# Kernel tuning notes

Hardware: AMD Instinct MI355X
Metric: run time of the kernel (lower is better)

## Reference

```python
import jax, jax.numpy as jnp
import numpy as np

HEADS = 8

def setup_inputs() -> dict:
    key = jax.random.key(0)
    ks = jax.random.split(key, 10)
    B, C, D, W, H = 4, 256, 12, 12, 12
    dk = C // HEADS
    return {
        "x": jax.random.normal(ks[0], (B, C, D, W, H), jnp.float32),
        "wq": jax.random.normal(ks[1], (C, C), jnp.float32) * 0.05,
        "bq": jax.random.normal(ks[2], (C,), jnp.float32) * 0.05,
        "wk": jax.random.normal(ks[3], (C, C), jnp.float32) * 0.05,
        "bk": jax.random.normal(ks[4], (C,), jnp.float32) * 0.05,
        "wv": jax.random.normal(ks[5], (C, C), jnp.float32) * 0.05,
        "bv": jax.random.normal(ks[6], (C,), jnp.float32) * 0.05,
        "rel_d": jax.random.normal(ks[7], (1, HEADS, dk, D, 1, 1), jnp.float32),
        "rel_h": jax.random.normal(ks[8], (1, HEADS, dk, 1, 1, H), jnp.float32),
        "rel_w": jax.random.normal(ks[9], (1, HEADS, dk, 1, W, 1), jnp.float32),
    }


def reference(x, wq, bq, wk, bk, wv, bv, rel_d, rel_h, rel_w):
    B, C, D, W, H = x.shape
    dk = C // HEADS
    N = D * W * H

    def proj(w, b):
        # Conv3d kernel_size=1 == per-voxel linear over channels
        y = jnp.einsum('bcdwh,oc->bodwh', x, w) + b[None, :, None, None, None]
        return y.reshape(B, HEADS, dk, N)  # [B,h,dk,N]

    q = proj(wq, bq)
    k = proj(wk, bk)
    v = proj(wv, bv)

    # content-content: q^T k -> [B,h,N,N]
    cc = jnp.einsum('bhdn,bhdm->bhnm', q, k)
    # relative-position bias: (rel_h+rel_w+rel_d) broadcasts to [1,h,dk,D,W,H]
    pos = (rel_h + rel_w + rel_d).reshape(1, HEADS, dk, N)
    # content-position: pos^T @ q -> [B,h,N,N]
    cp = jnp.einsum('bhdn,bhdm->bhnm', pos, q)

    attn = jax.nn.softmax(cc + cp, axis=-1)  # [B,h,N,N]
    # out = v @ attn^T -> [B,h,dk,N]
    out = jnp.einsum('bhdn,bhmn->bhdm', v, attn)
    return out.reshape(B, C, D, W, H)
```

## Files before the change

kernel.cpp:

```cpp
#include <hip/hip_runtime.h>
#include <math.h>

#define HEADS 8
#define DK 32
#define B_ 4
#define C_ 256
#define NVOX 1728
#define DE 64
#define PITCH 72
#define XPITCH 136
#define CPITCH 36
#define LOG2E 1.44269504088896f

typedef _Float16 f16x8 __attribute__((ext_vector_type(8)));
typedef __fp16 fp16x2 __attribute__((ext_vector_type(2)));
typedef float f32x16 __attribute__((ext_vector_type(16)));

__device__ inline float h2f(short s) {
    _Float16 h = *(_Float16*)&s;
    return (float)h;
}
__device__ inline f32x16 mfma32h(f16x8 a, f16x8 b, f32x16 c) {
    return __builtin_amdgcn_mfma_f32_32x32x16_f16(a, b, c, 0, 0, 0);
}

union H8 { _Float16 h[8]; uint4 v; };
union H4 { _Float16 h[4]; uint2 v; };

__global__ __launch_bounds__(256)
void prep_kernel(const float* __restrict__ x,
                 const float* __restrict__ wq, const float* __restrict__ wk,
                 const float* __restrict__ wv,
                 const float* __restrict__ rel_d, const float* __restrict__ rel_h,
                 const float* __restrict__ rel_w,
                 short* __restrict__ wf, short* __restrict__ xf,
                 short* __restrict__ Qf) {
    __shared__ float tile[64][65];
    int bid = blockIdx.x;
    int t = threadIdx.x;

    if (bid < 192) {
        int idx = (bid * 256 + t) * 4;
        int m = idx >> 16;
        const float* w = (m == 0) ? wq : (m == 1) ? wk : wv;
        float4 v = *(const float4*)&w[idx & 65535];
        H4 hh;
        hh.h[0] = (_Float16)v.x; hh.h[1] = (_Float16)v.y;
        hh.h[2] = (_Float16)v.z; hh.h[3] = (_Float16)v.w;
        *(uint2*)&wf[idx] = hh.v;
    } else if (bid < 624) {
        int q = bid - 192;
        int nb = (q % 27) * 64;
        int c0 = ((q / 27) % 4) * 64;
        int b  = q / 108;
        const float* xb = x + (size_t)b * C_ * NVOX;
        for (int e = t; e < 4096; e += 256) {
            int ci = e >> 6, nl = e & 63;
            tile[ci][nl] = xb[(size_t)(c0 + ci) * NVOX + nb + nl];
        }
        __syncthreads();
        for (int e = t; e < 512; e += 256) {
            int n = e >> 3, cg = (e & 7) * 8;
            H8 hi;
            #pragma unroll
            for (int j = 0; j < 8; j++) hi.h[j] = (_Float16)tile[cg + j][n];
            *(uint4*)&xf[((size_t)b * NVOX + nb + n) * C_ + c0 + cg] = hi.v;
        }
    } else {
        int q = bid - 624;
        int nb = (q % 27) * 64;
        int h  = (q / 27) % 8;
        int b  = q / 216;
        int bh = b * HEADS + h;
        int nl = t & 63, dd0 = (t >> 6) * 8;
        int n = nb + nl;
        int di = n / 144, wi = (n / 12) % 12, hi = n % 12;
        H8 ph;
        #pragma unroll
        for (int o = 0; o < 8; o++) {
            int hd = h * DK + dd0 + o;
            ph.h[o] = (_Float16)(rel_d[hd * 12 + di] + rel_w[hd * 12 + wi] +
                                 rel_h[hd * 12 + hi]);
        }
        *(uint4*)&Qf[((size_t)bh * NVOX + n) * DE + DK + dd0] = ph.v;
    }
}

struct FS {
    union {
        short xs[64 * XPITCH];
        float cbuf[3][64][CPITCH];
    } u;
};

__global__ __launch_bounds__(384, 4)
void fproj_kernel(const short* __restrict__ xf, const short* __restrict__ wf,
                  const float* __restrict__ bq, const float* __restrict__ bk,
                  const float* __restrict__ bv,
                  short* __restrict__ Qf, short* __restrict__ Kf,
                  short* __restrict__ Vf) {
    __shared__ FS sm;
    int nb = blockIdx.x * 64, h = blockIdx.y, b = blockIdx.z;
    int bh = b * HEADS + h;
    int t = threadIdx.x;
    int w = t >> 6, l = t & 63, ln = l & 31, hv = l >> 5;
    int mat = w >> 1, nh = w & 1;

    const short* xb = xf + ((size_t)b * NVOX + nb) * C_;
    const short* wA = wf + ((size_t)mat * C_ + h * DK + ln) * C_;
    int xrow = (nh * 32 + ln) * XPITCH;

    f32x16 acc;
    #pragma unroll
    for (int r = 0; r < 16; r++) acc[r] = 0.f;

    #pragma unroll 1
    for (int ch = 0; ch < 2; ch++) {
        __syncthreads();
        for (int e = t; e < 1024; e += 384) {
            int row = e >> 4, c8 = (e & 15) * 8;
            *(uint4*)&sm.u.xs[row * XPITCH + c8] =
                *(const uint4*)&xb[row * C_ + ch * 128 + c8];
        }
        __syncthreads();
        #pragma unroll 4
        for (int ks = 0; ks < 8; ks++) {
            int kl_ = ks * 16 + hv * 8;
            f16x8 a = *(const f16x8*)&wA[ch * 128 + kl_];
            f16x8 bfr = *(const f16x8*)&sm.u.xs[xrow + kl_];
            acc = mfma32h(a, bfr, acc);
        }
    }
    __syncthreads();

    const float* bias = (mat == 0) ? bq : (mat == 1) ? bk : bv;
    int ncol = nh * 32 + ln;
    #pragma unroll
    for (int q2 = 0; q2 < 4; q2++) {
        float4 cv;
        float* cvp = (float*)&cv;
        #pragma unroll
        for (int m = 0; m < 4; m++) {
            int o_loc = 8 * q2 + 4 * hv + m;
            cvp[m] = acc[4 * q2 + m] + bias[h * DK + o_loc];
        }
        *(float4*)&sm.u.cbuf[mat][ncol][8 * q2 + 4 * hv] = cv;
    }
    __syncthreads();

    if (t < 256) {
        int n = t >> 2, ddg = (t & 3) * 8;
        size_t rowoff = ((size_t)bh * NVOX + nb + n) * DE;
        H8 qh, kh;
        #pragma unroll
        for (int j = 0; j < 8; j++) {
            qh.h[j] = (_Float16)sm.u.cbuf[0][n][ddg + j];
            kh.h[j] = (_Float16)sm.u.cbuf[1][n][ddg + j];
        }
        *(uint4*)&Qf[rowoff + ddg] = qh.v;
        *(uint4*)&Kf[rowoff + ddg] = kh.v;
        *(uint4*)&Kf[rowoff + DK + ddg] = qh.v;
    }
    if (t < 256) {
        int d = t >> 3, ng = (t & 7) * 8;
        H8 vv;
        #pragma unroll
        for (int j = 0; j < 8; j++)
            vv.h[j] = (_Float16)sm.u.cbuf[2][ng + j][d];
        *(uint4*)&Vf[((size_t)bh * DK + d) * NVOX + nb + ng] = vv.v;
    }
}

struct SMem {
    short K[64][PITCH];
    short V[DK][PITCH];
    short P[64][PITCH];
};

__global__ __launch_bounds__(128, 3)
void attn_kernel(const short* __restrict__ Qf, const short* __restrict__ Kf,
                 const short* __restrict__ Vf,
                 short* __restrict__ wsO, float* __restrict__ wsM,
                 float* __restrict__ wsL) {
    __shared__ SMem sm;
    int bx = blockIdx.x;
    int it = bx >> 1, jp = bx & 1;
    int h = blockIdx.y, b = blockIdx.z;
    int bh = b * HEADS + h;
    int t = threadIdx.x;
    int w  = t >> 6;
    int l  = t & 63;
    int ln = l & 31;
    int hv = l >> 5;
    int i_loc  = w * 32 + ln;
    int i_glob = it * 64 + i_loc;

    const short* Qp = Qf + (size_t)bh * NVOX * DE;
    const short* Kp = Kf + (size_t)bh * NVOX * DE;
    const short* Vp = Vf + (size_t)bh * DK * NVOX;

    f16x8 qf[4];
    #pragma unroll
    for (int ks = 0; ks < 4; ks++)
        qf[ks] = *(const f16x8*)&Qp[(size_t)i_glob * DE + ks * 16 + hv * 8];

    float mL = -INFINITY;
    float lsum = 0.f;
    f32x16 O;
    #pragma unroll
    for (int r = 0; r < 16; r++) O[r] = 0.f;

    int krow0 = t >> 3, kcol = (t & 7) * 8;
    int vrow0 = t >> 3;
    uint4 kr[4], vr[2];

    int jt0 = jp ? 14 : 0, jt1 = jp ? 27 : 14;

    {
        int jb = jt0 * 64;
        #pragma unroll
        for (int q = 0; q < 4; q++)
            kr[q] = *(const uint4*)&Kp[(size_t)(jb + krow0 + q * 16) * DE + kcol];
        #pragma unroll
        for (int q = 0; q < 2; q++)
            vr[q] = *(const uint4*)&Vp[(size_t)(vrow0 + q * 16) * NVOX + jb + kcol];
        #pragma unroll
        for (int q = 0; q < 4; q++)
            *(uint4*)&sm.K[krow0 + q * 16][kcol] = kr[q];
        #pragma unroll
        for (int q = 0; q < 2; q++)
            *(uint4*)&sm.V[vrow0 + q * 16][kcol] = vr[q];
    }

    #pragma unroll 1
    for (int jt = jt0; jt < jt1; jt++) {
        __syncthreads();
        bool more = (jt + 1 < jt1);
        if (more) {
            int jb = (jt + 1) * 64;
            #pragma unroll
            for (int q = 0; q < 4; q++)
                kr[q] = *(const uint4*)&Kp[(size_t)(jb + krow0 + q * 16) * DE + kcol];
            #pragma unroll
            for (int q = 0; q < 2; q++)
                vr[q] = *(const uint4*)&Vp[(size_t)(vrow0 + q * 16) * NVOX + jb + kcol];
        }

        f32x16 sc[2];
        #pragma unroll
        for (int js = 0; js < 2; js++) {
            f32x16 s;
            #pragma unroll
            for (int r = 0; r < 16; r++) s[r] = 0.f;
            #pragma unroll
            for (int ks = 0; ks < 4; ks++) {
                f16x8 kfr = *(const f16x8*)&sm.K[js * 32 + ln][ks * 16 + hv * 8];
                s = mfma32h(kfr, qf[ks], s);
            }
            sc[js] = s;
        }

        float mx = sc[0][0];
        #pragma unroll
        for (int js = 0; js < 2; js++)
            #pragma unroll
            for (int r = 0; r < 16; r++) mx = fmaxf(mx, sc[js][r]);
        mx = fmaxf(mx, __shfl_xor(mx, 32));
        float mLn = fmaxf(mL, mx * LOG2E);
        float alpha = exp2f(mL - mLn);
        mL = mLn;
        float ps = 0.f;
        #pragma unroll
        for (int js = 0; js < 2; js++)
            #pragma unroll
            for (int r = 0; r < 16; r++) {
                float p = exp2f(fmaf(sc[js][r], LOG2E, -mLn));
                sc[js][r] = p;
                ps += p;
            }
        ps += __shfl_xor(ps, 32);
        lsum = lsum * alpha + ps;

        #pragma unroll
        for (int js = 0; js < 2; js++)
            #pragma unroll
            for (int g = 0; g < 4; g++) {
                union { fp16x2 h2[2]; uint2 v; } pk;
                pk.h2[0] = __builtin_amdgcn_cvt_pkrtz(sc[js][4 * g + 0], sc[js][4 * g + 1]);
                pk.h2[1] = __builtin_amdgcn_cvt_pkrtz(sc[js][4 * g + 2], sc[js][4 * g + 3]);
                *(uint2*)&sm.P[i_loc][js * 32 + g * 8 + hv * 4] = pk.v;
            }

        #pragma unroll
        for (int r = 0; r < 16; r++) O[r] *= alpha;
        #pragma unroll
        for (int ks = 0; ks < 4; ks++) {
            f16x8 va = *(const f16x8*)&sm.V[ln][ks * 16 + hv * 8];
            f16x8 pb = *(const f16x8*)&sm.P[i_loc][ks * 16 + hv * 8];
            O = mfma32h(va, pb, O);
        }

        __syncthreads();
        if (more) {
            #pragma unroll
            for (int q = 0; q < 4; q++)
                *(uint4*)&sm.K[krow0 + q * 16][kcol] = kr[q];
            #pragma unroll
            for (int q = 0; q < 2; q++)
                *(uint4*)&sm.V[vrow0 + q * 16][kcol] = vr[q];
        }
    }

    short* Op = wsO + ((size_t)jp * (B_ * HEADS) + bh) * DK * NVOX;
    #pragma unroll
    for (int r = 0; r < 16; r++) {
        int d = (r & 3) + 8 * (r >> 2) + 4 * hv;
        _Float16 oh = (_Float16)O[r];
        Op[(size_t)d * NVOX + i_glob] = *(short*)&oh;
    }
    if (hv == 0) {
        size_t mo = ((size_t)jp * (B_ * HEADS) + bh) * NVOX + i_glob;
        wsM[mo] = mL;
        wsL[mo] = lsum;
    }
}

__global__ void combine_kernel(const short* __restrict__ wsO,
                               const float* __restrict__ wsM,
                               const float* __restrict__ wsL,
                               float* __restrict__ out) {
    int idx = (blockIdx.x * 256 + threadIdx.x) * 4;
    int i = idx % NVOX;
    int bh = (idx / NVOX) >> 5;
    const size_t oh = (size_t)B_ * HEADS * DK * NVOX;
    const size_t mh = (size_t)B_ * HEADS * NVOX;
    size_t mo = (size_t)bh * NVOX + i;
    float4 m0 = *(const float4*)&wsM[mo];
    float4 m1 = *(const float4*)&wsM[mh + mo];
    float4 l0 = *(const float4*)&wsL[mo];
    float4 l1 = *(const float4*)&wsL[mh + mo];
    uint2 o0u = *(const uint2*)&wsO[idx];
    uint2 o1u = *(const uint2*)&wsO[oh + idx];
    const short* o0s = (const short*)&o0u;
    const short* o1s = (const short*)&o1u;
    const float* m0p = (const float*)&m0; const float* m1p = (const float*)&m1;
    const float* l0p = (const float*)&l0; const float* l1p = (const float*)&l1;
    float4 res;
    float* rp = (float*)&res;
    #pragma unroll
    for (int j = 0; j < 4; j++) {
        float m = fmaxf(m0p[j], m1p[j]);
        float a0 = exp2f(m0p[j] - m), a1 = exp2f(m1p[j] - m);
        rp[j] = (a0 * h2f(o0s[j]) + a1 * h2f(o1s[j])) /
                (a0 * l0p[j] + a1 * l1p[j]);
    }
    *(float4*)&out[idx] = res;
}

extern "C" void kernel_launch(void* const* d_in, const int* in_sizes, int n_in,
                              void* d_out, int out_size, void* d_ws, size_t ws_size,
                              hipStream_t stream) {
    const float* x     = (const float*)d_in[0];
    const float* wq    = (const float*)d_in[1];
    const float* bq    = (const float*)d_in[2];
    const float* wk    = (const float*)d_in[3];
    const float* bk    = (const float*)d_in[4];
    const float* wv    = (const float*)d_in[5];
    const float* bv    = (const float*)d_in[6];
    const float* rel_d = (const float*)d_in[7];
    const float* rel_h = (const float*)d_in[8];
    const float* rel_w = (const float*)d_in[9];
    float* out = (float*)d_out;

    size_t qksz = (size_t)B_ * HEADS * NVOX * DE;
    size_t vsz  = (size_t)B_ * HEADS * DK * NVOX;
    short* Qf  = (short*)d_ws;
    short* Kf  = Qf + qksz;
    short* Vf  = Kf + qksz;
    short* wf  = Vf + vsz;
    short* wsO = wf + (size_t)3 * C_ * C_;
    float* wsM = (float*)(wsO + 2 * vsz);
    float* wsL = wsM + 2 * (size_t)B_ * HEADS * NVOX;
    short* xf  = wsO;

    prep_kernel<<<dim3(1488), dim3(256), 0, stream>>>(
        x, wq, wk, wv, rel_d, rel_h, rel_w, wf, xf, Qf);
    fproj_kernel<<<dim3(NVOX / 64, HEADS, B_), dim3(384), 0, stream>>>(
        xf, wf, bq, bk, bv, Qf, Kf, Vf);
    attn_kernel<<<dim3(2 * NVOX / 64, HEADS, B_), dim3(128), 0, stream>>>(
        Qf, Kf, Vf, wsO, wsM, wsL);
    combine_kernel<<<dim3((int)(vsz / 1024)), dim3(256), 0, stream>>>(wsO, wsM, wsL, out);
}
```

Baseline: 187.6 us.

## Stop duplicating Q into K buffer and load key tiles directly per iteration

The projection kernel no longer writes a second copy of Q into the upper half of each K row. K is stored with DK width only. The attention kernel builds its 64-wide key tile in shared memory by reading the K half from Kf and the Q half from Qf. This cuts projection write traffic and workspace size. In exchange, the register-prefetch double buffering is removed: each tile is now loaded and synchronized before compute, so global load latency is no longer overlapped with MFMA work.

```diff
diff --git a/kernel.cpp b/kernel.cpp
--- a/kernel.cpp
+++ b/kernel.cpp
@@ -150,16 +150,14 @@
 
     if (t < 256) {
         int n = t >> 2, ddg = (t & 3) * 8;
-        size_t rowoff = ((size_t)bh * NVOX + nb + n) * DE;
         H8 qh, kh;
         #pragma unroll
         for (int j = 0; j < 8; j++) {
             qh.h[j] = (_Float16)sm.u.cbuf[0][n][ddg + j];
             kh.h[j] = (_Float16)sm.u.cbuf[1][n][ddg + j];
         }
-        *(uint4*)&Qf[rowoff + ddg] = qh.v;
-        *(uint4*)&Kf[rowoff + ddg] = kh.v;
-        *(uint4*)&Kf[rowoff + DK + ddg] = qh.v;
+        *(uint4*)&Qf[((size_t)bh * NVOX + nb + n) * DE + ddg] = qh.v;
+        *(uint4*)&Kf[((size_t)bh * NVOX + nb + n) * DK + ddg] = kh.v;
     }
     if (t < 256) {
         int d = t >> 3, ng = (t & 7) * 8;
@@ -196,7 +194,7 @@
     int i_glob = it * 64 + i_loc;
 
     const short* Qp = Qf + (size_t)bh * NVOX * DE;
-    const short* Kp = Kf + (size_t)bh * NVOX * DE;
+    const short* Kp = Kf + (size_t)bh * NVOX * DK;
     const short* Vp = Vf + (size_t)bh * DK * NVOX;
 
     f16x8 qf[4];
@@ -210,41 +208,23 @@
     #pragma unroll
     for (int r = 0; r < 16; r++) O[r] = 0.f;
 
-    int krow0 = t >> 3, kcol = (t & 7) * 8;
-    int vrow0 = t >> 3;
-    uint4 kr[4], vr[2];
-
     int jt0 = jp ? 14 : 0, jt1 = jp ? 27 : 14;
-
-    {
-        int jb = jt0 * 64;
-        #pragma unroll
-        for (int q = 0; q < 4; q++)
-            kr[q] = *(const uint4*)&Kp[(size_t)(jb + krow0 + q * 16) * DE + kcol];
-        #pragma unroll
-        for (int q = 0; q < 2; q++)
-            vr[q] = *(const uint4*)&Vp[(size_t)(vrow0 + q * 16) * NVOX + jb + kcol];
-        #pragma unroll
-        for (int q = 0; q < 4; q++)
-            *(uint4*)&sm.K[krow0 + q * 16][kcol] = kr[q];
-        #pragma unroll
-        for (int q = 0; q < 2; q++)
-            *(uint4*)&sm.V[vrow0 + q * 16][kcol] = vr[q];
-    }
-
     #pragma unroll 1
     for (int jt = jt0; jt < jt1; jt++) {
-        __syncthreads();
-        bool more = (jt + 1 < jt1);
-        if (more) {
-            int jb = (jt + 1) * 64;
-            #pragma unroll
-            for (int q = 0; q < 4; q++)
-                kr[q] = *(const uint4*)&Kp[(size_t)(jb + krow0 + q * 16) * DE + kcol];
-            #pragma unroll
-            for (int q = 0; q < 2; q++)
-                vr[q] = *(const uint4*)&Vp[(size_t)(vrow0 + q * 16) * NVOX + jb + kcol];
-        }
+        int jb = jt * 64;
+        __syncthreads();
+        for (int e = t; e < 512; e += 128) {
+            int row = e >> 3, cq = e & 7, c8 = cq * 8;
+            uint4 v = (cq < 4)
+                ? *(const uint4*)&Kp[(size_t)(jb + row) * DK + c8]
+                : *(const uint4*)&Qp[(size_t)(jb + row) * DE + (c8 - 32)];
+            *(uint4*)&sm.K[row][c8] = v;
+        }
+        for (int e = t; e < 256; e += 128) {
+            int d = e >> 3, c = (e & 7) * 8;
+            *(uint4*)&sm.V[d][c] = *(const uint4*)&Vp[(size_t)d * NVOX + jb + c];
+        }
+        __syncthreads();
 
         f32x16 sc[2];
         #pragma unroll
@@ -298,16 +278,6 @@
             f16x8 va = *(const f16x8*)&sm.V[ln][ks * 16 + hv * 8];
             f16x8 pb = *(const f16x8*)&sm.P[i_loc][ks * 16 + hv * 8];
             O = mfma32h(va, pb, O);
-        }
-
-        __syncthreads();
-        if (more) {
-            #pragma unroll
-            for (int q = 0; q < 4; q++)
-                *(uint4*)&sm.K[krow0 + q * 16][kcol] = kr[q];
-            #pragma unroll
-            for (int q = 0; q < 2; q++)
-                *(uint4*)&sm.V[vrow0 + q * 16][kcol] = vr[q];
         }
     }
 
@@ -376,7 +346,7 @@
     size_t vsz  = (size_t)B_ * HEADS * DK * NVOX;
     short* Qf  = (short*)d_ws;
     short* Kf  = Qf + qksz;
-    short* Vf  = Kf + qksz;
+    short* Vf  = Kf + vsz;
     short* wf  = Vf + vsz;
     short* wsO = wf + (size_t)3 * C_ * C_;
     float* wsM = (float*)(wsO + 2 * vsz);
```

Result: faster. 158.9 us (-15.3%).
